# Performance work log

Measured on AMD Instinct MI355X. Metric: run time of the kernel, lower is better.

The kernel has to match this reference:

```python
import jax, jax.numpy as jnp
import numpy as np

NUM_HEADS = 8
GS = 7  # group_size (window) side

def _relative_position_index():
    # static index table, matches the torch meshgrid('ij') construction
    coords = np.stack(np.meshgrid(np.arange(GS), np.arange(GS), indexing='ij'))  # (2,GS,GS)
    cf = coords.reshape(2, -1)                                 # (2, 49)
    rel = cf[:, :, None] - cf[:, None, :]                      # (2, 49, 49)
    rel = rel.transpose(1, 2, 0).copy()                        # (49, 49, 2)
    rel[..., 0] += GS - 1
    rel[..., 1] += GS - 1
    rel[..., 0] *= 2 * GS - 1
    return rel.sum(-1)                                         # (49, 49) in [0, 169)

REL_INDEX = jnp.asarray(_relative_position_index())

def setup_inputs() -> dict:
    key = jax.random.key(0)
    ks = jax.random.split(key, 5)
    B, N, C = 2048, 49, 256
    HID = 64
    return {
        'q': jax.random.normal(ks[0], (B, N, C), dtype=jnp.float32),
        'k': jax.random.normal(ks[1], (B, N, C), dtype=jnp.float32),
        'v': jax.random.normal(ks[2], (B, N, C), dtype=jnp.float32),
        'W1': jax.random.normal(ks[3], (2, HID), dtype=jnp.float32) * 0.1,
        'b1': jnp.zeros((HID,), dtype=jnp.float32),
        'W2': jax.random.normal(ks[4], (HID, NUM_HEADS), dtype=jnp.float32) * 0.1,
        'b2': jnp.zeros((NUM_HEADS,), dtype=jnp.float32),
        'H': 56,
        'W': 56,
    }

def _bias_table(W1, b1, W2, b2):
    # biases: (2*GS-1)^2 relative offsets, dpb_pos modeled as 2-layer MLP 2->HID->heads
    r = jnp.arange(1 - GS, GS, dtype=jnp.float32)
    bh, bw = jnp.meshgrid(r, r, indexing='ij')
    biases = jnp.stack([bh.ravel(), bw.ravel()], axis=1)       # (169, 2)
    pos = jax.nn.relu(biases @ W1 + b1) @ W2 + b2              # (169, heads)
    return pos[REL_INDEX].transpose(2, 0, 1)                   # (heads, 49, 49)

def reference(q, k, v, W1, b1, W2, b2, H, W):
    B, N, C = q.shape
    h = NUM_HEADS
    d = C // h
    scale = d ** -0.5
    qh = q.reshape(B, N, h, d)
    kh = k.reshape(B, N, h, d)
    vh = v.reshape(B, N, h, d)
    attn = jnp.einsum('bihd,bjhd->bhij', qh, kh) * scale       # (B,h,N,N)
    bias = _bias_table(W1, b1, W2, b2)                         # (h,49,49)
    if H == 7 and W == 7:
        attn = attn.at[:, :, 0:GS * GS, 0:GS * GS].add(bias[None])
    else:
        attn = attn + bias[None]
    attn = jax.nn.softmax(attn, axis=-1)
    out = jnp.einsum('bhij,bjhd->bihd', attn, vh).reshape(B, N, C)
    return out
```

## Files before the change

kernel.cpp:

```cpp
#include <hip/hip_runtime.h>
#include <hip/hip_bf16.h>

typedef __attribute__((ext_vector_type(8))) short bf16x8;
typedef __attribute__((ext_vector_type(4))) float f32x4;

#define NWIN 49
#define NH 8
#define CCH 256
#define PROW 72

__device__ __forceinline__ ushort2 pk_bf16(float a, float b) {
    __hip_bfloat162 t = __float22bfloat162_rn(float2{a, b});
    return *(ushort2*)&t;
}
__device__ __forceinline__ float upk(ushort u) { return __uint_as_float((unsigned)u << 16); }

__global__ void pos_mlp_kernel(const float* __restrict__ W1, const float* __restrict__ b1,
                               const float* __restrict__ W2, const float* __restrict__ b2,
                               float* __restrict__ pos) {
    int idx = blockIdx.x * blockDim.x + threadIdx.x;
    if (idx >= 169) return;
    float bh = (float)(idx / 13) - 6.0f;
    float bw = (float)(idx % 13) - 6.0f;
    float outv[NH];
#pragma unroll
    for (int t = 0; t < NH; ++t) outv[t] = b2[t];
    for (int u = 0; u < 64; ++u) {
        float hv = fmaf(bh, W1[u], fmaf(bw, W1[64 + u], b1[u]));
        hv = fmaxf(hv, 0.0f);
#pragma unroll
        for (int t = 0; t < NH; ++t) outv[t] = fmaf(hv, W2[u * NH + t], outv[t]);
    }
#pragma unroll
    for (int t = 0; t < NH; ++t) pos[idx * NH + t] = outv[t];
}

__global__ void bias_frag_kernel(const float* __restrict__ pos, float* __restrict__ bfrag) {
    int blk = blockIdx.x;
    int it = blk & 3, jt = (blk >> 2) & 3, h = blk >> 4;
    int lane = threadIdx.x;
    int g = lane >> 4, l15 = lane & 15;
    int i = it * 16 + l15;
    float4 v;
    float* vp = (float*)&v;
#pragma unroll
    for (int r = 0; r < 4; ++r) {
        int j = jt * 16 + g * 4 + r;
        float val;
        if (j >= NWIN) val = -1e30f;
        else if (i >= NWIN) val = 0.0f;
        else {
            int rel = (i / 7 - j / 7 + 6) * 13 + (i % 7 - j % 7 + 6);
            val = pos[rel * NH + h] * 1.4426950408889634f;
        }
        vp[r] = val;
    }
    *(float4*)(bfrag + (size_t)blk * 256 + lane * 4) = v;
}

__global__ __launch_bounds__(512, 4) void attn_kernel(
    const float* __restrict__ q, const float* __restrict__ k,
    const float* __restrict__ v, const float* __restrict__ bfrag,
    float* __restrict__ out) {
    __shared__ __align__(16) ushort sP[8][64 * PROW];

    const int nper = (int)(gridDim.x >> 3);
    const int b = ((int)blockIdx.x & 7) * nper + ((int)blockIdx.x >> 3);

    const int tid = threadIdx.x;
    const int w = tid >> 6, lane = tid & 63;
    const int h = w;
    const int g = lane >> 4, l15 = lane & 15;
    const size_t base = (size_t)b * (NWIN * CCH) + h * 32;
    ushort* myP = sP[w];

    bf16x8 kah[4], kal[4], qbh[4], qbl[4];
#pragma unroll
    for (int t = 0; t < 4; ++t) {
        int row = t * 16 + l15;
        int rc = row < NWIN ? row : NWIN - 1;
        const float* kp = k + base + (size_t)rc * CCH + g * 8;
        const float* qp = q + base + (size_t)rc * CCH + g * 8;
        float4 ka = *(const float4*)kp, kb = *(const float4*)(kp + 4);
        float4 qa = *(const float4*)qp, qb = *(const float4*)(qp + 4);
        ushort2 kh0 = pk_bf16(ka.x, ka.y), kh1 = pk_bf16(ka.z, ka.w);
        ushort2 kh2 = pk_bf16(kb.x, kb.y), kh3 = pk_bf16(kb.z, kb.w);
        ushort2 kl0 = pk_bf16(ka.x - upk(kh0.x), ka.y - upk(kh0.y));
        ushort2 kl1 = pk_bf16(ka.z - upk(kh1.x), ka.w - upk(kh1.y));
        ushort2 kl2 = pk_bf16(kb.x - upk(kh2.x), kb.y - upk(kh2.y));
        ushort2 kl3 = pk_bf16(kb.z - upk(kh3.x), kb.w - upk(kh3.y));
        ushort tkh[8] = {kh0.x, kh0.y, kh1.x, kh1.y, kh2.x, kh2.y, kh3.x, kh3.y};
        ushort tkl[8] = {kl0.x, kl0.y, kl1.x, kl1.y, kl2.x, kl2.y, kl3.x, kl3.y};
        kah[t] = *(bf16x8*)tkh; kal[t] = *(bf16x8*)tkl;
        ushort2 qh0 = pk_bf16(qa.x, qa.y), qh1 = pk_bf16(qa.z, qa.w);
        ushort2 qh2 = pk_bf16(qb.x, qb.y), qh3 = pk_bf16(qb.z, qb.w);
        ushort2 ql0 = pk_bf16(qa.x - upk(qh0.x), qa.y - upk(qh0.y));
        ushort2 ql1 = pk_bf16(qa.z - upk(qh1.x), qa.w - upk(qh1.y));
        ushort2 ql2 = pk_bf16(qb.x - upk(qh2.x), qb.y - upk(qh2.y));
        ushort2 ql3 = pk_bf16(qb.z - upk(qh3.x), qb.w - upk(qh3.y));
        ushort tqh[8] = {qh0.x, qh0.y, qh1.x, qh1.y, qh2.x, qh2.y, qh3.x, qh3.y};
        ushort tql[8] = {ql0.x, ql0.y, ql1.x, ql1.y, ql2.x, ql2.y, ql3.x, ql3.y};
        qbh[t] = *(bf16x8*)tqh; qbl[t] = *(bf16x8*)tql;
    }

    f32x4 acc[4][4];
#pragma unroll
    for (int jt = 0; jt < 4; ++jt)
#pragma unroll
        for (int it = 0; it < 4; ++it) {
            f32x4 a = {0.f, 0.f, 0.f, 0.f};
            a = __builtin_amdgcn_mfma_f32_16x16x32_bf16(kah[jt], qbh[it], a, 0, 0, 0);
            a = __builtin_amdgcn_mfma_f32_16x16x32_bf16(kah[jt], qbl[it], a, 0, 0, 0);
            a = __builtin_amdgcn_mfma_f32_16x16x32_bf16(kal[jt], qbh[it], a, 0, 0, 0);
            acc[jt][it] = a;
        }

    const float scale2 = 0.17677669529663687f * 1.4426950408889634f;
#pragma unroll
    for (int it = 0; it < 4; ++it) {
        float p[16];
        float s = 0.0f;
#pragma unroll
        for (int jt = 0; jt < 4; ++jt) {
            f32x4 bb = *(const f32x4*)(bfrag + (size_t)((h * 4 + jt) * 4 + it) * 256 + lane * 4);
#pragma unroll
            for (int r = 0; r < 4; ++r) {
                float e = __builtin_amdgcn_exp2f(fmaf(acc[jt][it][r], scale2, bb[r]));
                p[jt * 4 + r] = e;
                s += e;
            }
        }
        s += __shfl_xor(s, 16);
        s += __shfl_xor(s, 32);
        const float inv = 1.0f / s;
#pragma unroll
        for (int jt = 0; jt < 4; ++jt) {
            ushort2 a01 = pk_bf16(p[jt * 4 + 0] * inv, p[jt * 4 + 1] * inv);
            ushort2 a23 = pk_bf16(p[jt * 4 + 2] * inv, p[jt * 4 + 3] * inv);
            ushort4 w4; w4.x = a01.x; w4.y = a01.y; w4.z = a23.x; w4.w = a23.y;
            *(ushort4*)&myP[(it * 16 + l15) * PROW + jt * 16 + g * 4] = w4;
        }
    }

    bf16x8 bv[2][2];
#pragma unroll
    for (int ks = 0; ks < 2; ++ks)
#pragma unroll
        for (int nt = 0; nt < 2; ++nt) {
            float vv[8];
#pragma unroll
            for (int e = 0; e < 8; ++e) {
                int j = ks * 32 + g * 8 + e;
                int jc = j < NWIN ? j : NWIN - 1;
                vv[e] = v[base + (size_t)jc * CCH + nt * 16 + l15];
            }
            ushort2 p0 = pk_bf16(vv[0], vv[1]), p1 = pk_bf16(vv[2], vv[3]);
            ushort2 p2 = pk_bf16(vv[4], vv[5]), p3 = pk_bf16(vv[6], vv[7]);
            ushort tv[8] = {p0.x, p0.y, p1.x, p1.y, p2.x, p2.y, p3.x, p3.y};
            bv[ks][nt] = *(bf16x8*)tv;
        }

    f32x4 oacc[4][2];
#pragma unroll
    for (int mt = 0; mt < 4; ++mt)
#pragma unroll
        for (int nt = 0; nt < 2; ++nt) oacc[mt][nt] = (f32x4){0.f, 0.f, 0.f, 0.f};
#pragma unroll
    for (int ks = 0; ks < 2; ++ks)
#pragma unroll
        for (int mt = 0; mt < 4; ++mt) {
            bf16x8 pa = *(const bf16x8*)&myP[(mt * 16 + l15) * PROW + ks * 32 + g * 8];
#pragma unroll
            for (int nt = 0; nt < 2; ++nt)
                oacc[mt][nt] = __builtin_amdgcn_mfma_f32_16x16x32_bf16(pa, bv[ks][nt], oacc[mt][nt], 0, 0, 0);
        }

#pragma unroll
    for (int mt = 0; mt < 4; ++mt)
#pragma unroll
        for (int r = 0; r < 4; ++r) {
            int i = mt * 16 + g * 4 + r;
            if (i < NWIN) {
                float* op = out + base + (size_t)i * CCH + l15;
                op[0]  = oacc[mt][0][r];
                op[16] = oacc[mt][1][r];
            }
        }
}

extern "C" void kernel_launch(void* const* d_in, const int* in_sizes, int n_in,
                              void* d_out, int out_size, void* d_ws, size_t ws_size,
                              hipStream_t stream) {
    const float* q  = (const float*)d_in[0];
    const float* k  = (const float*)d_in[1];
    const float* v  = (const float*)d_in[2];
    const float* W1 = (const float*)d_in[3];
    const float* b1 = (const float*)d_in[4];
    const float* W2 = (const float*)d_in[5];
    const float* b2 = (const float*)d_in[6];

    float* pos   = (float*)d_ws;
    float* bfrag = (float*)((char*)d_ws + 8192);
    float* out   = (float*)d_out;

    const int B = in_sizes[0] / (NWIN * CCH);

    pos_mlp_kernel<<<1, 192, 0, stream>>>(W1, b1, W2, b2, pos);
    bias_frag_kernel<<<128, 64, 0, stream>>>(pos, bfrag);
    attn_kernel<<<B, 512, 0, stream>>>(q, k, v, bfrag, out);
}
```

Baseline: 105.1 us.

## Switch attention MFMAs to single-pass fp16 and hoist all global loads upfront

Replaces the three-pass bf16 hi/lo split QK^T product with a single fp16 MFMA. P and V also move from bf16 to fp16, converted with packed round-toward-zero conversions. Loads of K, Q, V and the bias fragments are all issued at kernel start, with empty asm barriers keeping them in registers so memory latency overlaps compute. Occupancy in launch bounds drops from 4 to 2 to make room for the extra live registers, and fp16 with round-toward-zero adds precision and range risk on large inputs.

Result: slower. 111.0 us (+5.6%).

```diff
diff --git a/kernel.cpp b/kernel.cpp
--- a/kernel.cpp
+++ b/kernel.cpp
@@ -1,7 +1,7 @@
 #include <hip/hip_runtime.h>
 #include <hip/hip_bf16.h>
 
-typedef __attribute__((ext_vector_type(8))) short bf16x8;
+typedef __attribute__((ext_vector_type(8))) _Float16 f16x8;
 typedef __attribute__((ext_vector_type(4))) float f32x4;
 
 #define NWIN 49
@@ -9,11 +9,20 @@
 #define CCH 256
 #define PROW 72
 
-__device__ __forceinline__ ushort2 pk_bf16(float a, float b) {
-    __hip_bfloat162 t = __float22bfloat162_rn(float2{a, b});
-    return *(ushort2*)&t;
-}
-__device__ __forceinline__ float upk(ushort u) { return __uint_as_float((unsigned)u << 16); }
+__device__ __forceinline__ uint cvt2_u32(float a, float b) {
+    auto t = __builtin_amdgcn_cvt_pkrtz(a, b);
+    return *(uint*)&t;
+}
+__device__ __forceinline__ f16x8 mk8(uint a, uint b, uint c, uint d) {
+    union { uint u[4]; f16x8 v; } x;
+    x.u[0] = a; x.u[1] = b; x.u[2] = c; x.u[3] = d;
+    return x.v;
+}
+__device__ __forceinline__ ushort4 pack4(uint a, uint b) {
+    union { uint u[2]; ushort4 s; } x;
+    x.u[0] = a; x.u[1] = b;
+    return x.s;
+}
 
 __global__ void pos_mlp_kernel(const float* __restrict__ W1, const float* __restrict__ b1,
                                const float* __restrict__ W2, const float* __restrict__ b2,
@@ -58,7 +67,7 @@
     *(float4*)(bfrag + (size_t)blk * 256 + lane * 4) = v;
 }
 
-__global__ __launch_bounds__(512, 4) void attn_kernel(
+__global__ __launch_bounds__(512, 2) void attn_kernel(
     const float* __restrict__ q, const float* __restrict__ k,
     const float* __restrict__ v, const float* __restrict__ bfrag,
     float* __restrict__ out) {
@@ -74,33 +83,48 @@
     const size_t base = (size_t)b * (NWIN * CCH) + h * 32;
     ushort* myP = sP[w];
 
-    bf16x8 kah[4], kal[4], qbh[4], qbl[4];
+    float4 kraw[4][2], qraw[4][2];
 #pragma unroll
     for (int t = 0; t < 4; ++t) {
         int row = t * 16 + l15;
         int rc = row < NWIN ? row : NWIN - 1;
         const float* kp = k + base + (size_t)rc * CCH + g * 8;
         const float* qp = q + base + (size_t)rc * CCH + g * 8;
-        float4 ka = *(const float4*)kp, kb = *(const float4*)(kp + 4);
-        float4 qa = *(const float4*)qp, qb = *(const float4*)(qp + 4);
-        ushort2 kh0 = pk_bf16(ka.x, ka.y), kh1 = pk_bf16(ka.z, ka.w);
-        ushort2 kh2 = pk_bf16(kb.x, kb.y), kh3 = pk_bf16(kb.z, kb.w);
-        ushort2 kl0 = pk_bf16(ka.x - upk(kh0.x), ka.y - upk(kh0.y));
-        ushort2 kl1 = pk_bf16(ka.z - upk(kh1.x), ka.w - upk(kh1.y));
-        ushort2 kl2 = pk_bf16(kb.x - upk(kh2.x), kb.y - upk(kh2.y));
-        ushort2 kl3 = pk_bf16(kb.z - upk(kh3.x), kb.w - upk(kh3.y));
-        ushort tkh[8] = {kh0.x, kh0.y, kh1.x, kh1.y, kh2.x, kh2.y, kh3.x, kh3.y};
-        ushort tkl[8] = {kl0.x, kl0.y, kl1.x, kl1.y, kl2.x, kl2.y, kl3.x, kl3.y};
-        kah[t] = *(bf16x8*)tkh; kal[t] = *(bf16x8*)tkl;
-        ushort2 qh0 = pk_bf16(qa.x, qa.y), qh1 = pk_bf16(qa.z, qa.w);
-        ushort2 qh2 = pk_bf16(qb.x, qb.y), qh3 = pk_bf16(qb.z, qb.w);
-        ushort2 ql0 = pk_bf16(qa.x - upk(qh0.x), qa.y - upk(qh0.y));
-        ushort2 ql1 = pk_bf16(qa.z - upk(qh1.x), qa.w - upk(qh1.y));
-        ushort2 ql2 = pk_bf16(qb.x - upk(qh2.x), qb.y - upk(qh2.y));
-        ushort2 ql3 = pk_bf16(qb.z - upk(qh3.x), qb.w - upk(qh3.y));
-        ushort tqh[8] = {qh0.x, qh0.y, qh1.x, qh1.y, qh2.x, qh2.y, qh3.x, qh3.y};
-        ushort tql[8] = {ql0.x, ql0.y, ql1.x, ql1.y, ql2.x, ql2.y, ql3.x, ql3.y};
-        qbh[t] = *(bf16x8*)tqh; qbl[t] = *(bf16x8*)tql;
+        kraw[t][0] = *(const float4*)kp; kraw[t][1] = *(const float4*)(kp + 4);
+        qraw[t][0] = *(const float4*)qp; qraw[t][1] = *(const float4*)(qp + 4);
+    }
+    float vv[2][2][8];
+#pragma unroll
+    for (int ks = 0; ks < 2; ++ks)
+#pragma unroll
+        for (int nt = 0; nt < 2; ++nt)
+#pragma unroll
+            for (int e = 0; e < 8; ++e) {
+                int j = ks * 32 + g * 8 + e;
+                int jc = j < NWIN ? j : NWIN - 1;
+                vv[ks][nt][e] = v[base + (size_t)jc * CCH + nt * 16 + l15];
+            }
+    f32x4 bb[4][4];
+#pragma unroll
+    for (int jt = 0; jt < 4; ++jt)
+#pragma unroll
+        for (int it = 0; it < 4; ++it)
+            bb[jt][it] = *(const f32x4*)(bfrag + (size_t)((h * 4 + jt) * 4 + it) * 256 + lane * 4);
+
+#pragma unroll
+    for (int t = 0; t < 4; ++t)
+        asm volatile("" :: "v"(kraw[t][0].x), "v"(kraw[t][1].x),
+                           "v"(qraw[t][0].x), "v"(qraw[t][1].x));
+
+    f16x8 ka16[4], qb16[4];
+#pragma unroll
+    for (int t = 0; t < 4; ++t) {
+        float4 a = kraw[t][0], c = kraw[t][1];
+        ka16[t] = mk8(cvt2_u32(a.x, a.y), cvt2_u32(a.z, a.w),
+                      cvt2_u32(c.x, c.y), cvt2_u32(c.z, c.w));
+        float4 d = qraw[t][0], e = qraw[t][1];
+        qb16[t] = mk8(cvt2_u32(d.x, d.y), cvt2_u32(d.z, d.w),
+                      cvt2_u32(e.x, e.y), cvt2_u32(e.z, e.w));
     }
 
     f32x4 acc[4][4];
@@ -109,11 +133,13 @@
 #pragma unroll
         for (int it = 0; it < 4; ++it) {
             f32x4 a = {0.f, 0.f, 0.f, 0.f};
-            a = __builtin_amdgcn_mfma_f32_16x16x32_bf16(kah[jt], qbh[it], a, 0, 0, 0);
-            a = __builtin_amdgcn_mfma_f32_16x16x32_bf16(kah[jt], qbl[it], a, 0, 0, 0);
-            a = __builtin_amdgcn_mfma_f32_16x16x32_bf16(kal[jt], qbh[it], a, 0, 0, 0);
-            acc[jt][it] = a;
-        }
+            acc[jt][it] = __builtin_amdgcn_mfma_f32_16x16x32_f16(ka16[jt], qb16[it], a, 0, 0, 0);
+        }
+
+#pragma unroll
+    for (int jt = 0; jt < 4; ++jt)
+        asm volatile("" :: "v"(bb[jt][0].x), "v"(bb[jt][1].x),
+                           "v"(bb[jt][2].x), "v"(bb[jt][3].x));
 
     const float scale2 = 0.17677669529663687f * 1.4426950408889634f;
 #pragma unroll
@@ -121,44 +147,41 @@
         float p[16];
         float s = 0.0f;
 #pragma unroll
-        for (int jt = 0; jt < 4; ++jt) {
-            f32x4 bb = *(const f32x4*)(bfrag + (size_t)((h * 4 + jt) * 4 + it) * 256 + lane * 4);
+        for (int jt = 0; jt < 4; ++jt)
 #pragma unroll
             for (int r = 0; r < 4; ++r) {
-                float e = __builtin_amdgcn_exp2f(fmaf(acc[jt][it][r], scale2, bb[r]));
+                float e = __builtin_amdgcn_exp2f(fmaf(acc[jt][it][r], scale2, bb[jt][it][r]));
                 p[jt * 4 + r] = e;
                 s += e;
             }
-        }
         s += __shfl_xor(s, 16);
         s += __shfl_xor(s, 32);
         const float inv = 1.0f / s;
 #pragma unroll
         for (int jt = 0; jt < 4; ++jt) {
-            ushort2 a01 = pk_bf16(p[jt * 4 + 0] * inv, p[jt * 4 + 1] * inv);
-            ushort2 a23 = pk_bf16(p[jt * 4 + 2] * inv, p[jt * 4 + 3] * inv);
-            ushort4 w4; w4.x = a01.x; w4.y = a01.y; w4.z = a23.x; w4.w = a23.y;
-            *(ushort4*)&myP[(it * 16 + l15) * PROW + jt * 16 + g * 4] = w4;
-        }
-    }
-
-    bf16x8 bv[2][2];
-#pragma unroll
-    for (int ks = 0; ks < 2; ++ks)
-#pragma unroll
-        for (int nt = 0; nt < 2; ++nt) {
-            float vv[8];
-#pragma unroll
-            for (int e = 0; e < 8; ++e) {
-                int j = ks * 32 + g * 8 + e;
-                int jc = j < NWIN ? j : NWIN - 1;
-                vv[e] = v[base + (size_t)jc * CCH + nt * 16 + l15];
-            }
-            ushort2 p0 = pk_bf16(vv[0], vv[1]), p1 = pk_bf16(vv[2], vv[3]);
-            ushort2 p2 = pk_bf16(vv[4], vv[5]), p3 = pk_bf16(vv[6], vv[7]);
-            ushort tv[8] = {p0.x, p0.y, p1.x, p1.y, p2.x, p2.y, p3.x, p3.y};
-            bv[ks][nt] = *(bf16x8*)tv;
-        }
+            uint a01 = cvt2_u32(p[jt * 4 + 0] * inv, p[jt * 4 + 1] * inv);
+            uint a23 = cvt2_u32(p[jt * 4 + 2] * inv, p[jt * 4 + 3] * inv);
+            *(ushort4*)&myP[(it * 16 + l15) * PROW + jt * 16 + g * 4] = pack4(a01, a23);
+        }
+    }
+
+#pragma unroll
+    for (int ks = 0; ks < 2; ++ks)
+#pragma unroll
+        for (int nt = 0; nt < 2; ++nt)
+            asm volatile("" :: "v"(vv[ks][nt][0]), "v"(vv[ks][nt][1]),
+                               "v"(vv[ks][nt][2]), "v"(vv[ks][nt][3]),
+                               "v"(vv[ks][nt][4]), "v"(vv[ks][nt][5]),
+                               "v"(vv[ks][nt][6]), "v"(vv[ks][nt][7]));
+    f16x8 bv[2][2];
+#pragma unroll
+    for (int ks = 0; ks < 2; ++ks)
+#pragma unroll
+        for (int nt = 0; nt < 2; ++nt)
+            bv[ks][nt] = mk8(cvt2_u32(vv[ks][nt][0], vv[ks][nt][1]),
+                             cvt2_u32(vv[ks][nt][2], vv[ks][nt][3]),
+                             cvt2_u32(vv[ks][nt][4], vv[ks][nt][5]),
+                             cvt2_u32(vv[ks][nt][6], vv[ks][nt][7]));
 
     f32x4 oacc[4][2];
 #pragma unroll
@@ -169,10 +192,10 @@
     for (int ks = 0; ks < 2; ++ks)
 #pragma unroll
         for (int mt = 0; mt < 4; ++mt) {
-            bf16x8 pa = *(const bf16x8*)&myP[(mt * 16 + l15) * PROW + ks * 32 + g * 8];
+            f16x8 pa = *(const f16x8*)&myP[(mt * 16 + l15) * PROW + ks * 32 + g * 8];
 #pragma unroll
             for (int nt = 0; nt < 2; ++nt)
-                oacc[mt][nt] = __builtin_amdgcn_mfma_f32_16x16x32_bf16(pa, bv[ks][nt], oacc[mt][nt], 0, 0, 0);
+                oacc[mt][nt] = __builtin_amdgcn_mfma_f32_16x16x32_f16(pa, bv[ks][nt], oacc[mt][nt], 0, 0, 0);
         }
 
 #pragma unroll
```
